# Performance work log

Hardware: AMD Instinct MI355X
Metric: run time of the kernel (lower is better)

The kernel has to match this reference:

```python
import jax, jax.numpy as jnp
import numpy as np

N = 50000       # nodes
F_IN = 256
F_OUT = 64
H = 4           # heads
DEG = 16        # avg degree (random edges per node)
NEG_SLOPE = 0.2


def setup_inputs() -> dict:
    key = jax.random.key(0)
    k_h, k_e, k_w, k_fc = jax.random.split(key, 4)
    h = jax.random.normal(k_h, (N, F_IN), dtype=jnp.float32)
    # random edges + explicit self-loops so every node has >= 1 out-edge
    e_rand = jax.random.randint(k_e, (2, N * DEG), 0, N, dtype=jnp.int64)
    loops = jnp.tile(jnp.arange(N, dtype=jnp.int64)[None, :], (2, 1))
    edge_index = jnp.concatenate([e_rand, loops], axis=1)  # [2, 850000]
    # Glorot-uniform-like scales
    s_w = np.sqrt(6.0 / (F_IN + F_OUT)).astype(np.float32)
    s_a = np.sqrt(6.0 / (2 * F_OUT + 1)).astype(np.float32)
    w = jax.random.uniform(k_w, (H, F_IN, F_OUT), jnp.float32, -s_w, s_w)
    fc = jax.random.uniform(k_fc, (H, 2 * F_OUT, 1), jnp.float32, -s_a, s_a)
    bias = jnp.zeros((F_OUT,), jnp.float32)
    return {"h": h, "edge_index": edge_index, "w": w, "fc": fc, "bias": bias}


def reference(h, edge_index, w, fc, bias):
    # GAT forward, vectorized over edges (dropout is identity at inference).
    n = h.shape[0]
    f_out = w.shape[2]
    src, dst = edge_index[0], edge_index[1]           # [E]
    h_prime = jnp.einsum('nf,hfo->hno', h, w)          # [H, N, F]
    a = fc[..., 0]                                     # [H, 2F]
    a_src, a_dst = a[:, :f_out], a[:, f_out:]          # [H, F] each
    s_src = jnp.einsum('hnf,hf->hn', h_prime, a_src)   # [H, N] score of center node
    s_dst = jnp.einsum('hnf,hf->hn', h_prime, a_dst)   # [H, N] score of neighbor
    e = jax.nn.leaky_relu(s_src[:, src] + s_dst[:, dst], NEG_SLOPE)  # [H, E]
    e = e.T                                            # [E, H]
    # segment softmax over edges grouped by source node
    seg_max = jax.ops.segment_max(e, src, num_segments=n)   # [N, H]
    ex = jnp.exp(e - seg_max[src])                           # [E, H]
    denom = jax.ops.segment_sum(ex, src, num_segments=n)    # [N, H]
    alpha = ex / denom[src]                                  # [E, H]
    # scatter-aggregate: out_i = sum_{j in N(i)} alpha_ij * Wh_j
    msgs = alpha[:, :, None] * jnp.transpose(h_prime[:, dst, :], (1, 0, 2))  # [E, H, F]
    out = jax.ops.segment_sum(msgs, src, num_segments=n)    # [N, H, F]
    return out.mean(axis=1) + bias                           # [N, F]
```

## Files before the change

### kernel.cpp

```cpp
#include <hip/hip_runtime.h>
#include <cfloat>

#define FIN 256
#define FOUT 64
#define NH 4
#define NEG_SLOPE 0.2f
#define SLOTS 64
#define BCAP 3072
#define P1T 4096

typedef __bf16 bf16x8 __attribute__((ext_vector_type(8)));
typedef float f32x4 __attribute__((ext_vector_type(4)));

__device__ __forceinline__ ushort f2bf(float f) {
    return (ushort)((__float_as_uint(f) + 0x8000u) >> 16);
}
__device__ __forceinline__ float bf2f(ushort u) {
    return __uint_as_float(((unsigned)u) << 16);
}
__device__ __forceinline__ float lrelu(float x) {
    return (x >= 0.f) ? x : NEG_SLOPE * x;
}

__global__ __launch_bounds__(256) void k1(
    const int* __restrict__ ei, int E, int nbuck,
    int* __restrict__ gcur,
    unsigned* __restrict__ barea,
    const float* __restrict__ w, ushort* __restrict__ wt, int p1B)
{
    __shared__ int lcnt[512];
    __shared__ int lbase[512];

    if ((int)blockIdx.x >= p1B) {
        const int g = ((int)blockIdx.x - p1B) * 256 + threadIdx.x;
        const int hh  = g >> 14;
        const int rem = g & 16383;
        const int c   = rem >> 8;
        const int k   = rem & 255;
        wt[g] = f2bf(w[(((hh << 8) | k) << 6) | c]);
        return;
    }

    const int tid = threadIdx.x;
    for (int b = tid; b < nbuck; b += 256) lcnt[b] = 0;
    __syncthreads();

    const int e0 = (int)blockIdx.x * P1T;
    int s[16], d[16];
#pragma unroll
    for (int i = 0; i < 16; ++i) {
        const int e = e0 + i * 256 + tid;
        if (e < E) {
            s[i] = ei[e];
            d[i] = ei[E + e];
            atomicAdd(&lcnt[s[i] >> 7], 1);
        } else {
            s[i] = -1; d[i] = 0;
        }
    }
    __syncthreads();
    for (int b = tid; b < nbuck; b += 256) {
        const int c = lcnt[b];
        lbase[b] = c ? atomicAdd(&gcur[b * 16], c) : 0;
        lcnt[b] = 0;
    }
    __syncthreads();
#pragma unroll
    for (int i = 0; i < 16; ++i) {
        if (s[i] >= 0) {
            const int b = s[i] >> 7;
            const int r = atomicAdd(&lcnt[b], 1);
            const int pos = lbase[b] + r;
            if (pos < BCAP)
                barea[(size_t)b * BCAP + pos] =
                    ((unsigned)(s[i] & 127) << 16) | (unsigned)d[i];
        }
    }
}

#define ASTRIDE 280
#define OSTRIDE 260
__global__ __launch_bounds__(256) void k2(
    const int* __restrict__ gcur, const unsigned* __restrict__ barea,
    ushort* __restrict__ col, int* __restrict__ cursor, int p2B,
    const float* __restrict__ h, const ushort* __restrict__ wt,
    const float* __restrict__ fc, ushort* __restrict__ hp,
    float* __restrict__ s_src, float* __restrict__ s_dst, int N)
{
    __shared__ ushort lds[64 * ASTRIDE];

    const int tid = threadIdx.x;

    if ((int)blockIdx.x < p2B) {
        ushort* colT = lds;
        int* cnt = (int*)(lds + 128 * SLOTS);
        const int b = blockIdx.x;
        for (int i = tid; i < 128; i += 256) cnt[i] = 0;
        __syncthreads();
        int c = gcur[b * 16];
        if (c > BCAP) c = BCAP;
        for (int j = tid; j < c; j += 256) {
            const unsigned p = barea[(size_t)b * BCAP + j];
            const int sl = (int)(p >> 16);
            const int r = atomicAdd(&cnt[sl], 1);
            if (r < SLOTS) colT[sl * SLOTS + r] = (ushort)(p & 0xFFFFu);
        }
        __syncthreads();
        const size_t gbase = (size_t)b * 128 * SLOTS;
        for (int idx = tid; idx < 128 * SLOTS / 4; idx += 256)
            *(ushort4*)&col[gbase + (size_t)idx * 4] =
                *(const ushort4*)&colT[idx * 4];
        for (int i = tid; i < 128; i += 256)
            cursor[b * 128 + i] = cnt[i];
        return;
    }

    const int bid = (int)blockIdx.x - p2B;
    const int n0 = bid * 64;

    for (int idx = tid; idx < 64 * 64; idx += 256) {
        const int row  = idx >> 6;
        const int quad = idx & 63;
        const int n = n0 + row;
        float4 v = make_float4(0.f, 0.f, 0.f, 0.f);
        if (n < N) v = ((const float4*)(h + (size_t)n * FIN))[quad];
        ushort4 bv;
        bv.x = f2bf(v.x); bv.y = f2bf(v.y); bv.z = f2bf(v.z); bv.w = f2bf(v.w);
        *(ushort4*)&lds[row * ASTRIDE + quad * 4] = bv;
    }
    __syncthreads();

    const int head = tid >> 6;
    const int lane = tid & 63;
    const int lrow = lane & 15;
    const int lq   = lane >> 4;

    const ushort* wth = wt + head * (64 * 256);

    f32x4 acc[4][4];
#pragma unroll
    for (int mt = 0; mt < 4; ++mt)
#pragma unroll
        for (int nt = 0; nt < 4; ++nt)
            acc[mt][nt] = (f32x4){0.f, 0.f, 0.f, 0.f};

#pragma unroll
    for (int kt = 0; kt < 8; ++kt) {
        const int kof = kt * 32 + lq * 8;
        bf16x8 af[4];
#pragma unroll
        for (int mt = 0; mt < 4; ++mt)
            af[mt] = *(const bf16x8*)&lds[(mt * 16 + lrow) * ASTRIDE + kof];
#pragma unroll
        for (int nt = 0; nt < 4; ++nt) {
            const bf16x8 bfr = *(const bf16x8*)&wth[(nt * 16 + lrow) * 256 + kof];
#pragma unroll
            for (int mt = 0; mt < 4; ++mt)
                acc[mt][nt] = __builtin_amdgcn_mfma_f32_16x16x32_bf16(
                    af[mt], bfr, acc[mt][nt], 0, 0, 0);
        }
    }

    float as_[4], ad_[4];
#pragma unroll
    for (int nt = 0; nt < 4; ++nt) {
        as_[nt] = fc[head * 2 * FOUT + nt * 16 + lrow];
        ad_[nt] = fc[head * 2 * FOUT + FOUT + nt * 16 + lrow];
    }
#pragma unroll
    for (int mt = 0; mt < 4; ++mt) {
        const int rbase = n0 + mt * 16 + lq * 4;
#pragma unroll
        for (int r = 0; r < 4; ++r) {
            const int n = rbase + r;
            float ps = 0.f, pd = 0.f;
#pragma unroll
            for (int nt = 0; nt < 4; ++nt) {
                const float v = acc[mt][nt][r];
                ps = fmaf(v, as_[nt], ps);
                pd = fmaf(v, ad_[nt], pd);
            }
            ps += __shfl_xor(ps, 1); pd += __shfl_xor(pd, 1);
            ps += __shfl_xor(ps, 2); pd += __shfl_xor(pd, 2);
            ps += __shfl_xor(ps, 4); pd += __shfl_xor(pd, 4);
            ps += __shfl_xor(ps, 8); pd += __shfl_xor(pd, 8);
            if (lrow == 0 && n < N) {
                s_src[(size_t)n * NH + head] = ps;
                s_dst[(size_t)n * NH + head] = pd;
            }
        }
    }

    __syncthreads();
#pragma unroll
    for (int mt = 0; mt < 4; ++mt)
#pragma unroll
        for (int r = 0; r < 4; ++r)
#pragma unroll
            for (int nt = 0; nt < 4; ++nt)
                lds[(mt * 16 + lq * 4 + r) * OSTRIDE +
                    (nt * 16 + lrow) * 4 + head] = f2bf(acc[mt][nt][r]);
    __syncthreads();
    for (int idx = tid; idx < 64 * 64; idx += 256) {
        const int row = idx >> 6;
        const int c   = idx & 63;
        const int n = n0 + row;
        if (n < N)
            *(ushort4*)&hp[(size_t)n * 256 + c * 4] =
                *(const ushort4*)&lds[row * OSTRIDE + c * 4];
    }
}

__global__ __launch_bounds__(256) void k_agg(
    const int* __restrict__ cursor, const ushort* __restrict__ col,
    const ushort* __restrict__ hp,
    const float* __restrict__ s_src, const float* __restrict__ s_dst,
    const float* __restrict__ bias, float* __restrict__ out, int N, int base)
{
    const int wid  = threadIdx.x >> 6;
    const int lane = threadIdx.x & 63;
    const int n    = base + blockIdx.x * 4 + wid;
    if (n >= N) return;

    const size_t start = (size_t)n * SLOTS;
    const int deg = min(cursor[n], SLOTS);
    const float4 ssn = ((const float4*)s_src)[n];
    const float4* sd4 = (const float4*)s_dst;

    float4 acc = make_float4(0.f, 0.f, 0.f, 0.f);

    int dreg = 0;
    float4 x = make_float4(-FLT_MAX, -FLT_MAX, -FLT_MAX, -FLT_MAX);
    if (lane < deg) {
        dreg = col[start + lane];
        const float4 sd = sd4[dreg];
        x.x = lrelu(ssn.x + sd.x);
        x.y = lrelu(ssn.y + sd.y);
        x.z = lrelu(ssn.z + sd.z);
        x.w = lrelu(ssn.w + sd.w);
    }
    float4 m = x;
#pragma unroll
    for (int d = 32; d; d >>= 1) {
        m.x = fmaxf(m.x, __shfl_xor(m.x, d));
        m.y = fmaxf(m.y, __shfl_xor(m.y, d));
        m.z = fmaxf(m.z, __shfl_xor(m.z, d));
        m.w = fmaxf(m.w, __shfl_xor(m.w, d));
    }
    float4 e = make_float4(0.f, 0.f, 0.f, 0.f);
    if (lane < deg) {
        e.x = __expf(x.x - m.x);
        e.y = __expf(x.y - m.y);
        e.z = __expf(x.z - m.z);
        e.w = __expf(x.w - m.w);
    }
    float4 s = e;
#pragma unroll
    for (int d = 32; d; d >>= 1) {
        s.x += __shfl_xor(s.x, d);
        s.y += __shfl_xor(s.y, d);
        s.z += __shfl_xor(s.z, d);
        s.w += __shfl_xor(s.w, d);
    }
    float4 alpha;
    alpha.x = e.x / s.x;
    alpha.y = e.y / s.y;
    alpha.z = e.z / s.z;
    alpha.w = e.w / s.w;

    const int nblk = (deg + 3) >> 2;
    for (int b = 0; b < nblk; ++b) {
        int dd[4]; float4 av[4]; ushort4 v[4];
#pragma unroll
        for (int u = 0; u < 4; ++u) {
            const int j = b * 4 + u;
            dd[u]   = __shfl(dreg, j);
            av[u].x = __shfl(alpha.x, j);
            av[u].y = __shfl(alpha.y, j);
            av[u].z = __shfl(alpha.z, j);
            av[u].w = __shfl(alpha.w, j);
        }
#pragma unroll
        for (int u = 0; u < 4; ++u)
            v[u] = *(const ushort4*)&hp[((size_t)dd[u] * FOUT + lane) * NH];
#pragma unroll
        for (int u = 0; u < 4; ++u) {
            acc.x = fmaf(av[u].x, bf2f(v[u].x), acc.x);
            acc.y = fmaf(av[u].y, bf2f(v[u].y), acc.y);
            acc.z = fmaf(av[u].z, bf2f(v[u].z), acc.z);
            acc.w = fmaf(av[u].w, bf2f(v[u].w), acc.w);
        }
    }

    out[(size_t)n * FOUT + lane] =
        (acc.x + acc.y + acc.z + acc.w) * 0.25f + bias[lane];
}

extern "C" void kernel_launch(void* const* d_in, const int* in_sizes, int n_in,
                              void* d_out, int out_size, void* d_ws, size_t ws_size,
                              hipStream_t stream)
{
    const float* h    = (const float*)d_in[0];
    const int*   ei   = (const int*)d_in[1];
    const float* w    = (const float*)d_in[2];
    const float* fc   = (const float*)d_in[3];
    const float* bias = (const float*)d_in[4];
    float* out = (float*)d_out;

    const int N = in_sizes[0] / FIN;
    const int E = in_sizes[1] / 2;
    const int nbuck = (N + 127) >> 7;

    char* ws = (char*)d_ws;
    auto take = [&](size_t bytes) {
        char* p = ws;
        ws += (bytes + 255) & ~(size_t)255;
        return p;
    };
    ushort*   wt      = (ushort*)take((size_t)NH * FIN * FOUT * sizeof(ushort));
    ushort*   h_prime = (ushort*)take((size_t)NH * N * FOUT * sizeof(ushort));
    float*    s_src   = (float*)take((size_t)NH * N * sizeof(float));
    float*    s_dst   = (float*)take((size_t)NH * N * sizeof(float));
    int*      cursor  = (int*)take((size_t)nbuck * 128 * sizeof(int));
    ushort*   col     = (ushort*)take((size_t)nbuck * 128 * SLOTS * sizeof(ushort));
    int*      gcur    = (int*)take((size_t)nbuck * 16 * sizeof(int));
    unsigned* barea   = (unsigned*)take((size_t)nbuck * BCAP * sizeof(unsigned));

    hipMemsetAsync(gcur, 0, (size_t)nbuck * 16 * sizeof(int), stream);

    const int p1B = (E + P1T - 1) / P1T;
    k1<<<p1B + 256, 256, 0, stream>>>(ei, E, nbuck, gcur, barea, w, wt, p1B);

    const int gemmB = (N + 63) / 64;
    k2<<<nbuck + gemmB, 256, 0, stream>>>(gcur, barea, col, cursor, nbuck,
                                          h, wt, fc, h_prime, s_src, s_dst, N);

    const int total_blocks = (N + 3) / 4;
    const int hb = total_blocks / 2;
    k_agg<<<hb, 256, 0, stream>>>(cursor, col, h_prime, s_src, s_dst,
                                  bias, out, N, 0);
    k_agg<<<total_blocks - hb, 256, 0, stream>>>(cursor, col, h_prime,
                                                 s_src, s_dst, bias, out, N, hb * 4);
}
```

Measured before the change: 149.9 us.

## Co-schedule edge bucketing with GEMM and split weight conversion into own kernel

The weight bf16 conversion moves to its own small kernel. The edge-bucketing pass now shares a launch with the projection GEMM, and the per-bucket CSR compaction runs as a separate kernel afterwards, so the memory-bound edge pass overlaps the compute-bound GEMM. The GEMM now batches the h loads into registers before converting them, and hoists the B-fragment loads ahead of the MFMA loop to expose more memory parallelism. This adds one extra kernel launch and more register pressure in the GEMM.

```diff
diff --git a/kernel.cpp b/kernel.cpp
--- a/kernel.cpp
+++ b/kernel.cpp
@@ -22,111 +22,94 @@
     return (x >= 0.f) ? x : NEG_SLOPE * x;
 }
 
+__global__ __launch_bounds__(256) void k0_wconv(const float* __restrict__ w,
+                                                ushort* __restrict__ wt)
+{
+    const int g = blockIdx.x * 256 + threadIdx.x;
+    const int hh  = g >> 14;
+    const int rem = g & 16383;
+    const int c   = rem >> 8;
+    const int k   = rem & 255;
+    wt[g] = f2bf(w[(((hh << 8) | k) << 6) | c]);
+}
+
+#define ASTRIDE 280
+#define OSTRIDE 260
 __global__ __launch_bounds__(256) void k1(
     const int* __restrict__ ei, int E, int nbuck,
-    int* __restrict__ gcur,
-    unsigned* __restrict__ barea,
-    const float* __restrict__ w, ushort* __restrict__ wt, int p1B)
-{
-    __shared__ int lcnt[512];
-    __shared__ int lbase[512];
-
-    if ((int)blockIdx.x >= p1B) {
-        const int g = ((int)blockIdx.x - p1B) * 256 + threadIdx.x;
-        const int hh  = g >> 14;
-        const int rem = g & 16383;
-        const int c   = rem >> 8;
-        const int k   = rem & 255;
-        wt[g] = f2bf(w[(((hh << 8) | k) << 6) | c]);
-        return;
-    }
-
-    const int tid = threadIdx.x;
-    for (int b = tid; b < nbuck; b += 256) lcnt[b] = 0;
-    __syncthreads();
-
-    const int e0 = (int)blockIdx.x * P1T;
-    int s[16], d[16];
-#pragma unroll
-    for (int i = 0; i < 16; ++i) {
-        const int e = e0 + i * 256 + tid;
-        if (e < E) {
-            s[i] = ei[e];
-            d[i] = ei[E + e];
-            atomicAdd(&lcnt[s[i] >> 7], 1);
-        } else {
-            s[i] = -1; d[i] = 0;
-        }
-    }
-    __syncthreads();
-    for (int b = tid; b < nbuck; b += 256) {
-        const int c = lcnt[b];
-        lbase[b] = c ? atomicAdd(&gcur[b * 16], c) : 0;
-        lcnt[b] = 0;
-    }
-    __syncthreads();
-#pragma unroll
-    for (int i = 0; i < 16; ++i) {
-        if (s[i] >= 0) {
-            const int b = s[i] >> 7;
-            const int r = atomicAdd(&lcnt[b], 1);
-            const int pos = lbase[b] + r;
-            if (pos < BCAP)
-                barea[(size_t)b * BCAP + pos] =
-                    ((unsigned)(s[i] & 127) << 16) | (unsigned)d[i];
-        }
-    }
-}
-
-#define ASTRIDE 280
-#define OSTRIDE 260
-__global__ __launch_bounds__(256) void k2(
-    const int* __restrict__ gcur, const unsigned* __restrict__ barea,
-    ushort* __restrict__ col, int* __restrict__ cursor, int p2B,
+    int* __restrict__ gcur, unsigned* __restrict__ barea, int p1B,
     const float* __restrict__ h, const ushort* __restrict__ wt,
     const float* __restrict__ fc, ushort* __restrict__ hp,
     float* __restrict__ s_src, float* __restrict__ s_dst, int N)
 {
     __shared__ ushort lds[64 * ASTRIDE];
-
     const int tid = threadIdx.x;
 
-    if ((int)blockIdx.x < p2B) {
-        ushort* colT = lds;
-        int* cnt = (int*)(lds + 128 * SLOTS);
-        const int b = blockIdx.x;
-        for (int i = tid; i < 128; i += 256) cnt[i] = 0;
+    if ((int)blockIdx.x < p1B) {
+        int* lcnt  = (int*)lds;
+        int* lbase = (int*)lds + 512;
+        for (int b = tid; b < nbuck; b += 256) lcnt[b] = 0;
         __syncthreads();
-        int c = gcur[b * 16];
-        if (c > BCAP) c = BCAP;
-        for (int j = tid; j < c; j += 256) {
-            const unsigned p = barea[(size_t)b * BCAP + j];
-            const int sl = (int)(p >> 16);
-            const int r = atomicAdd(&cnt[sl], 1);
-            if (r < SLOTS) colT[sl * SLOTS + r] = (ushort)(p & 0xFFFFu);
+
+        const int e0 = (int)blockIdx.x * P1T;
+        int s[16], d[16];
+#pragma unroll
+        for (int i = 0; i < 16; ++i) {
+            const int e = e0 + i * 256 + tid;
+            if (e < E) {
+                s[i] = ei[e];
+                d[i] = ei[E + e];
+                atomicAdd(&lcnt[s[i] >> 7], 1);
+            } else {
+                s[i] = -1; d[i] = 0;
+            }
         }
         __syncthreads();
-        const size_t gbase = (size_t)b * 128 * SLOTS;
-        for (int idx = tid; idx < 128 * SLOTS / 4; idx += 256)
-            *(ushort4*)&col[gbase + (size_t)idx * 4] =
-                *(const ushort4*)&colT[idx * 4];
-        for (int i = tid; i < 128; i += 256)
-            cursor[b * 128 + i] = cnt[i];
+        for (int b = tid; b < nbuck; b += 256) {
+            const int c = lcnt[b];
+            lbase[b] = c ? atomicAdd(&gcur[b * 16], c) : 0;
+            lcnt[b] = 0;
+        }
+        __syncthreads();
+#pragma unroll
+        for (int i = 0; i < 16; ++i) {
+            if (s[i] >= 0) {
+                const int b = s[i] >> 7;
+                const int r = atomicAdd(&lcnt[b], 1);
+                const int pos = lbase[b] + r;
+                if (pos < BCAP)
+                    barea[(size_t)b * BCAP + pos] =
+                        ((unsigned)(s[i] & 127) << 16) | (unsigned)d[i];
+            }
+        }
         return;
     }
 
-    const int bid = (int)blockIdx.x - p2B;
+    const int bid = (int)blockIdx.x - p1B;
     const int n0 = bid * 64;
 
-    for (int idx = tid; idx < 64 * 64; idx += 256) {
-        const int row  = idx >> 6;
-        const int quad = idx & 63;
-        const int n = n0 + row;
-        float4 v = make_float4(0.f, 0.f, 0.f, 0.f);
-        if (n < N) v = ((const float4*)(h + (size_t)n * FIN))[quad];
-        ushort4 bv;
-        bv.x = f2bf(v.x); bv.y = f2bf(v.y); bv.z = f2bf(v.z); bv.w = f2bf(v.w);
-        *(ushort4*)&lds[row * ASTRIDE + quad * 4] = bv;
+#pragma unroll
+    for (int half = 0; half < 2; ++half) {
+        float4 va[8];
+#pragma unroll
+        for (int i = 0; i < 8; ++i) {
+            const int idx = half * 2048 + i * 256 + tid;
+            const int row  = idx >> 6;
+            const int quad = idx & 63;
+            const int n = n0 + row;
+            va[i] = (n < N) ? ((const float4*)(h + (size_t)n * FIN))[quad]
+                            : make_float4(0.f, 0.f, 0.f, 0.f);
+        }
+#pragma unroll
+        for (int i = 0; i < 8; ++i) {
+            const int idx = half * 2048 + i * 256 + tid;
+            const int row  = idx >> 6;
+            const int quad = idx & 63;
+            ushort4 bv;
+            bv.x = f2bf(va[i].x); bv.y = f2bf(va[i].y);
+            bv.z = f2bf(va[i].z); bv.w = f2bf(va[i].w);
+            *(ushort4*)&lds[row * ASTRIDE + quad * 4] = bv;
+        }
     }
     __syncthreads();
 
@@ -147,18 +130,20 @@
 #pragma unroll
     for (int kt = 0; kt < 8; ++kt) {
         const int kof = kt * 32 + lq * 8;
+        bf16x8 bfr[4];
+#pragma unroll
+        for (int nt = 0; nt < 4; ++nt)
+            bfr[nt] = *(const bf16x8*)&wth[(nt * 16 + lrow) * 256 + kof];
         bf16x8 af[4];
 #pragma unroll
         for (int mt = 0; mt < 4; ++mt)
             af[mt] = *(const bf16x8*)&lds[(mt * 16 + lrow) * ASTRIDE + kof];
 #pragma unroll
-        for (int nt = 0; nt < 4; ++nt) {
-            const bf16x8 bfr = *(const bf16x8*)&wth[(nt * 16 + lrow) * 256 + kof];
+        for (int nt = 0; nt < 4; ++nt)
 #pragma unroll
             for (int mt = 0; mt < 4; ++mt)
                 acc[mt][nt] = __builtin_amdgcn_mfma_f32_16x16x32_bf16(
-                    af[mt], bfr, acc[mt][nt], 0, 0, 0);
-        }
+                    af[mt], bfr[nt], acc[mt][nt], 0, 0, 0);
     }
 
     float as_[4], ad_[4];
@@ -209,6 +194,33 @@
             *(ushort4*)&hp[(size_t)n * 256 + c * 4] =
                 *(const ushort4*)&lds[row * OSTRIDE + c * 4];
     }
+}
+
+__global__ __launch_bounds__(256) void k2(
+    const int* __restrict__ gcur, const unsigned* __restrict__ barea,
+    ushort* __restrict__ col, int* __restrict__ cursor)
+{
+    __shared__ ushort colT[128 * SLOTS];
+    __shared__ int cnt[128];
+    const int tid = threadIdx.x;
+    const int b = blockIdx.x;
+    for (int i = tid; i < 128; i += 256) cnt[i] = 0;
+    __syncthreads();
+    int c = gcur[b * 16];
+    if (c > BCAP) c = BCAP;
+    for (int j = tid; j < c; j += 256) {
+        const unsigned p = barea[(size_t)b * BCAP + j];
+        const int sl = (int)(p >> 16);
+        const int r = atomicAdd(&cnt[sl], 1);
+        if (r < SLOTS) colT[sl * SLOTS + r] = (ushort)(p & 0xFFFFu);
+    }
+    __syncthreads();
+    const size_t gbase = (size_t)b * 128 * SLOTS;
+    for (int idx = tid; idx < 128 * SLOTS / 4; idx += 256)
+        *(ushort4*)&col[gbase + (size_t)idx * 4] =
+            *(const ushort4*)&colT[idx * 4];
+    for (int i = tid; i < 128; i += 256)
+        cursor[b * 128 + i] = cnt[i];
 }
 
 __global__ __launch_bounds__(256) void k_agg(
@@ -328,12 +340,14 @@
 
     hipMemsetAsync(gcur, 0, (size_t)nbuck * 16 * sizeof(int), stream);
 
-    const int p1B = (E + P1T - 1) / P1T;
-    k1<<<p1B + 256, 256, 0, stream>>>(ei, E, nbuck, gcur, barea, w, wt, p1B);
-
+    k0_wconv<<<256, 256, 0, stream>>>(w, wt);
+
+    const int p1B   = (E + P1T - 1) / P1T;
     const int gemmB = (N + 63) / 64;
-    k2<<<nbuck + gemmB, 256, 0, stream>>>(gcur, barea, col, cursor, nbuck,
-                                          h, wt, fc, h_prime, s_src, s_dst, N);
+    k1<<<p1B + gemmB, 256, 0, stream>>>(ei, E, nbuck, gcur, barea, p1B,
+                                        h, wt, fc, h_prime, s_src, s_dst, N);
+
+    k2<<<nbuck, 256, 0, stream>>>(gcur, barea, col, cursor);
 
     const int total_blocks = (N + 3) / 4;
     const int hb = total_blocks / 2;
```

After: 142.1 us. -5.2%, faster.
